# Kernel optimization log

Hardware: AMD Instinct MI355X
Metric: run time of the kernel (lower is better)

## Reference

```python
import math
import jax, jax.numpy as jnp
import numpy as np

B, T, D, L, E = 2, 1024, 1024, 12, 4
EPS = 1e-5


def _ln(v, g, b):
    mu = jnp.mean(v, axis=-1, keepdims=True)
    var = jnp.mean(jnp.square(v - mu), axis=-1, keepdims=True)
    return (v - mu) * jax.lax.rsqrt(var + EPS) * g + b


def setup_inputs() -> dict:
    key = jax.random.key(0)
    ks = jax.random.split(key, 4)
    x = jax.random.normal(ks[0], (B, T, D), dtype=jnp.float32)
    queries = jax.random.normal(ks[1], (L, D), dtype=jnp.float32) * 0.02
    W1 = jax.random.normal(ks[2], (L, D, E * D), dtype=jnp.float32) * 0.02
    W2 = jax.random.normal(ks[3], (L, E * D, D), dtype=jnp.float32) * 0.02
    return {
        'x': x,
        'queries': queries,
        'kn_g': jnp.ones((L, D), jnp.float32),
        'kn_b': jnp.zeros((L, D), jnp.float32),
        'ln_g': jnp.ones((L, D), jnp.float32),
        'ln_b': jnp.zeros((L, D), jnp.float32),
        'W1': W1,
        'b1': jnp.zeros((L, E * D), jnp.float32),
        'W2': W2,
        'b2': jnp.zeros((L, D), jnp.float32),
    }


def reference(x, queries, kn_g, kn_b, ln_g, ln_b, W1, b1, W2, b2):
    scale = 1.0 / math.sqrt(D)
    history = [x]
    h = x
    for l in range(L):
        V = jnp.stack(history, axis=0)              # (l+1, B, T, D)
        K = _ln(V, kn_g[l], kn_b[l])
        scores = jnp.einsum('d,lbtd->lbt', queries[l], K) * scale
        alpha = jax.nn.softmax(scores, axis=0)       # softmax over history axis
        residual = jnp.einsum('lbt,lbtd->btd', alpha, V)
        u = _ln(h, ln_g[l], ln_b[l])
        ff = jax.nn.gelu(u @ W1[l] + b1[l], approximate=False) @ W2[l] + b2[l]
        h = residual + ff
        history.append(h)
    return h
```

## Files before the change

kernel.cpp:

```cpp
#include <hip/hip_runtime.h>
#include <math.h>

#define BATCH 2
#define TSEQ 1024
#define DIM 1024
#define NLAYER 12
#define EDIM 4096
#define BT 2048
#define EPS_LN 1e-5f

typedef __attribute__((ext_vector_type(4))) float  f32x4;
typedef __attribute__((ext_vector_type(8))) __bf16 bf16x8;
typedef __attribute__((ext_vector_type(4))) __bf16 bf16x4;

__device__ __forceinline__ void gl_lds16(const void* gptr, void* lptr) {
    __builtin_amdgcn_global_load_lds(
        (const __attribute__((address_space(1))) void*)gptr,
        (__attribute__((address_space(3))) void*)lptr,
        16, 0, 0);
}

__device__ __forceinline__ void wtile256(float (*t)[65], const float* src,
                                         __bf16* dst, int R, int C,
                                         int rt, int ct, int tid)
{
    int lr = tid >> 2, cs = (tid & 3) << 4;
    const float* sp = src + (size_t)(rt * 64 + lr) * C + ct * 64 + cs;
#pragma unroll
    for (int s = 0; s < 4; s++) {
        f32x4 v = *(const f32x4*)(sp + s * 4);
        t[lr][cs + s * 4 + 0] = v[0];
        t[lr][cs + s * 4 + 1] = v[1];
        t[lr][cs + s * 4 + 2] = v[2];
        t[lr][cs + s * 4 + 3] = v[3];
    }
    __syncthreads();
    int oc = tid >> 2, rs = (tid & 3) << 4;
    bf16x8 o0, o1;
#pragma unroll
    for (int e = 0; e < 8; e++) o0[e] = (__bf16)t[rs + e][oc];
#pragma unroll
    for (int e = 0; e < 8; e++) o1[e] = (__bf16)t[rs + 8 + e][oc];
    __bf16* dp = dst + (size_t)(ct * 64 + oc) * R + rt * 64 + rs;
    *(bf16x8*)dp = o0;
    *(bf16x8*)(dp + 8) = o1;
}

__global__ __launch_bounds__(256) void wtrans_kernel(
    const float* __restrict__ W1, const float* __restrict__ W2,
    __bf16* __restrict__ W1t, __bf16* __restrict__ W2t)
{
    __shared__ float t[64][65];
    int z = blockIdx.z;
    if (z == 0) wtile256(t, W1, W1t, DIM, EDIM, blockIdx.y, blockIdx.x, threadIdx.x);
    else        wtile256(t, W2, W2t, EDIM, DIM, blockIdx.x, blockIdx.y, threadIdx.x);
}

__global__ __launch_bounds__(256)
void attn_wt_kernel(const float* __restrict__ x,
                    const float* __restrict__ baseprev,
                    __bf16* __restrict__ histbf,
                    const __bf16* __restrict__ part,
                    const float* __restrict__ q,
                    const float* __restrict__ kng,
                    const float* __restrict__ knb,
                    const float* __restrict__ lng,
                    const float* __restrict__ lnb,
                    const float* __restrict__ b2,
                    float* __restrict__ hnext,
                    __bf16* __restrict__ u,
                    int nl,
                    const float* __restrict__ W1n,
                    const float* __restrict__ W2n,
                    __bf16* __restrict__ W1tn,
                    __bf16* __restrict__ W2tn,
                    int dowt)
{
    __shared__ char smem[49408];

    if (blockIdx.x >= BT) {
        if (!dowt) return;
        float (*t)[65] = (float(*)[65])smem;
        int tile = blockIdx.x - BT;
        if (tile < 1024) wtile256(t, W1n, W1tn, DIM, EDIM, tile >> 6, tile & 63, threadIdx.x);
        else { int t3 = tile - 1024; wtile256(t, W2n, W2tn, EDIM, DIM, t3 & 63, t3 >> 6, threadIdx.x); }
        return;
    }

    float (*V)[DIM] = (float(*)[DIM])smem;
    float* sS  = (float*)(smem + 49152);
    float* sMu = sS + NLAYER;
    float* sRs = sMu + NLAYER;

    const int bt = blockIdx.x;
    const int tid = threadIdx.x, lane = tid & 63, w = tid >> 6;

    f32x4 gqv[4];
    float sg = 0.f, sb = 0.f;
#pragma unroll
    for (int i = 0; i < 4; i++) {
        int d = i * 256 + lane * 4;
        f32x4 g4 = *(const f32x4*)(kng + d);
        f32x4 q4 = *(const f32x4*)(q + d);
        f32x4 b4 = *(const f32x4*)(knb + d);
#pragma unroll
        for (int c = 0; c < 4; c++) {
            float gq = g4[c] * q4[c];
            gqv[i][c] = gq;
            sg += gq;
            sb += b4[c] * q4[c];
        }
    }
#pragma unroll
    for (int off = 32; off; off >>= 1) {
        sg += __shfl_xor(sg, off);
        sb += __shfl_xor(sb, off);
    }

    for (int lp = w; lp < nl; lp += 4) {
        f32x4 vv[4];
        if (lp == nl - 1) {
            const float* vp = (nl == 1) ? (x + (size_t)bt * DIM)
                                        : (baseprev + (size_t)bt * DIM);
#pragma unroll
            for (int i = 0; i < 4; i++) vv[i] = *(const f32x4*)(vp + i * 256 + lane * 4);
            if (part) {
#pragma unroll
                for (int z = 0; z < 4; z++) {
                    const __bf16* pp = part + ((size_t)z * BT + bt) * DIM;
#pragma unroll
                    for (int i = 0; i < 4; i++) {
                        bf16x4 p4 = *(const bf16x4*)(pp + i * 256 + lane * 4);
#pragma unroll
                        for (int c = 0; c < 4; c++) vv[i][c] += (float)p4[c];
                    }
                }
            }
            if (nl < NLAYER) {
                __bf16* mp = histbf + ((size_t)lp * BT + bt) * DIM;
#pragma unroll
                for (int i = 0; i < 4; i++) {
                    bf16x4 m4;
#pragma unroll
                    for (int c = 0; c < 4; c++) m4[c] = (__bf16)vv[i][c];
                    *(bf16x4*)(mp + i * 256 + lane * 4) = m4;
                }
            }
        } else {
            const __bf16* mp = histbf + ((size_t)lp * BT + bt) * DIM;
#pragma unroll
            for (int i = 0; i < 4; i++) {
                bf16x4 m4 = *(const bf16x4*)(mp + i * 256 + lane * 4);
#pragma unroll
                for (int c = 0; c < 4; c++) vv[i][c] = (float)m4[c];
            }
        }

        float s1 = 0.f, s2 = 0.f, sq = 0.f;
#pragma unroll
        for (int i = 0; i < 4; i++) {
            *(f32x4*)(&V[lp][i * 256 + lane * 4]) = vv[i];
#pragma unroll
            for (int c = 0; c < 4; c++) {
                float xv = vv[i][c];
                s1 += xv; s2 += xv * xv; sq += xv * gqv[i][c];
            }
        }
#pragma unroll
        for (int off = 32; off; off >>= 1) {
            s1 += __shfl_xor(s1, off);
            s2 += __shfl_xor(s2, off);
            sq += __shfl_xor(sq, off);
        }
        if (lane == 0) {
            float mu = s1 * (1.0f / DIM);
            float var = s2 * (1.0f / DIM) - mu * mu;
            float rs = rsqrtf(var + EPS_LN);
            sMu[lp] = mu; sRs[lp] = rs;
            sS[lp] = (rs * (sq - mu * sg) + sb) * (1.0f / 32.0f);
        }
    }
    __syncthreads();

    float mx = -1e30f;
#pragma unroll
    for (int i = 0; i < NLAYER; i++) if (i < nl) mx = fmaxf(mx, sS[i]);
    float al[NLAYER];
    float ssum = 0.f;
#pragma unroll
    for (int i = 0; i < NLAYER; i++) {
        al[i] = (i < nl) ? __expf(sS[i] - mx) : 0.f;
        ssum += al[i];
    }
    float inv = 1.0f / ssum;

    const int d = tid * 4;
    f32x4 r; r[0] = 0.f; r[1] = 0.f; r[2] = 0.f; r[3] = 0.f;
#pragma unroll
    for (int i = 0; i < NLAYER; i++) {
        if (i < nl) {
            f32x4 v4 = *(const f32x4*)(&V[i][d]);
            float a = al[i] * inv;
            r[0] += a * v4[0]; r[1] += a * v4[1]; r[2] += a * v4[2]; r[3] += a * v4[3];
        }
    }
    f32x4 h4 = *(const f32x4*)(&V[nl - 1][d]);
    f32x4 b24 = *(const f32x4*)(b2 + d);
    f32x4 ro; ro[0] = r[0] + b24[0]; ro[1] = r[1] + b24[1];
    ro[2] = r[2] + b24[2]; ro[3] = r[3] + b24[3];
    *(f32x4*)(hnext + (size_t)bt * DIM + d) = ro;

    float mu = sMu[nl - 1], rs = sRs[nl - 1];
    f32x4 g4 = *(const f32x4*)(lng + d);
    f32x4 b4 = *(const f32x4*)(lnb + d);
    bf16x4 uo;
#pragma unroll
    for (int c = 0; c < 4; c++) uo[c] = (__bf16)((h4[c] - mu) * rs * g4[c] + b4[c]);
    *(bf16x4*)(u + (size_t)bt * DIM + d) = uo;
}

#define STG 49152

template <int EPI>
__global__ __launch_bounds__(512, 1)
void gemm8(const __bf16* __restrict__ A, const __bf16* __restrict__ Bt,
           const float* __restrict__ bias, void* __restrict__ outp,
           int N, int As, int Bs)
{
    __shared__ char lds[3 * STG];
    const int tid = threadIdx.x, lane = tid & 63, w = tid >> 6;
    const int wm = w >> 2, wn = w & 3;
    const int lr = lane & 15;
    const int hib = (lane >> 4) << 4;
    const int NT = 16;

    const int fid = blockIdx.x;
    const int m0 = (fid & 15) * 128;
    const int n0 = (fid >> 4) * 256;
    const int kbase = blockIdx.y * 1024;

    f32x4 acc[4][4];
#pragma unroll
    for (int i = 0; i < 4; i++)
#pragma unroll
        for (int j = 0; j < 4; j++) { acc[i][j][0]=0.f; acc[i][j][1]=0.f; acc[i][j][2]=0.f; acc[i][j][3]=0.f; }

    const int srow = tid >> 3;
    const int ksrc = ((tid & 7) << 4) ^ ((srow & 7) << 4);
    const char* Ac = (const char*)A;
    const char* Bc = (const char*)Bt;
    size_t aoff[2], boff[4];
#pragma unroll
    for (int c = 0; c < 2; c++)
        aoff[c] = ((size_t)(m0 + c * 64 + srow) * As + kbase) * 2 + ksrc;
#pragma unroll
    for (int c = 0; c < 4; c++)
        boff[c] = ((size_t)(n0 + c * 64 + srow) * Bs + kbase) * 2 + ksrc;

    char* abw = lds + w * 1024;
    char* bbw = lds + 16384 + w * 1024;

    auto STAGE = [&](int tt, int bi) {
        size_t kb = (size_t)tt * 128;
        char* ab = abw + bi * STG;
        char* bb = bbw + bi * STG;
#pragma unroll
        for (int c = 0; c < 2; c++) gl_lds16(Ac + aoff[c] + kb, ab + c * 8192);
#pragma unroll
        for (int c = 0; c < 4; c++) gl_lds16(Bc + boff[c] + kb, bb + c * 8192);
    };

    STAGE(0, 0);
    STAGE(1, 1);

    int sb = 0, st = 2;
#pragma unroll 1
    for (int t = 0; t < NT; ++t) {
        if (t < NT - 1) asm volatile("s_waitcnt vmcnt(6)" ::: "memory");
        else            asm volatile("s_waitcnt vmcnt(0)" ::: "memory");
        __builtin_amdgcn_s_barrier();
        __builtin_amdgcn_sched_barrier(0);

        if (t + 2 < NT) STAGE(t + 2, st);

        const char* base = lds + sb * STG;
        bf16x8 af[2][4], bfr[2][4];
#pragma unroll
        for (int kk = 0; kk < 2; kk++) {
#pragma unroll
            for (int i = 0; i < 4; i++) {
                int ra = wm * 64 + i * 16 + lr;
                af[kk][i] = *(const bf16x8*)(base + ra * 128 + ((kk * 64 + hib) ^ ((ra & 7) << 4)));
            }
#pragma unroll
            for (int j = 0; j < 4; j++) {
                int rb = wn * 64 + j * 16 + lr;
                bfr[kk][j] = *(const bf16x8*)(base + 16384 + rb * 128 + ((kk * 64 + hib) ^ ((rb & 7) << 4)));
            }
        }
        __builtin_amdgcn_s_setprio(1);
#pragma unroll
        for (int kk = 0; kk < 2; kk++)
#pragma unroll
            for (int i = 0; i < 4; i++)
#pragma unroll
                for (int j = 0; j < 4; j++)
                    acc[i][j] = __builtin_amdgcn_mfma_f32_16x16x32_bf16(af[kk][i], bfr[kk][j], acc[i][j], 0, 0, 0);
        __builtin_amdgcn_s_setprio(0);

        sb = (sb == 2) ? 0 : sb + 1;
        st = (st == 2) ? 0 : st + 1;
    }

    const int lrow = (lane >> 4) << 2;
    if (EPI == 0) {
        __bf16* out = (__bf16*)outp;
#pragma unroll
        for (int i = 0; i < 4; i++) {
#pragma unroll
            for (int j = 0; j < 4; j++) {
                int colg = n0 + wn * 64 + j * 16 + lr;
                float bc = bias[colg];
#pragma unroll
                for (int r = 0; r < 4; r++) {
                    int rowg = m0 + wm * 64 + i * 16 + lrow + r;
                    float v = acc[i][j][r] + bc;
                    float tt2 = 0.7978845608f * (v + 0.044715f * v * v * v);
                    float e = __expf(2.0f * tt2);
                    float th = 1.0f - 2.0f / (e + 1.0f);
                    out[(size_t)rowg * N + colg] = (__bf16)(0.5f * v * (1.0f + th));
                }
            }
        }
    } else {
        __bf16* out = (__bf16*)outp + (size_t)blockIdx.y * BT * N;
#pragma unroll
        for (int i = 0; i < 4; i++) {
#pragma unroll
            for (int j = 0; j < 4; j++) {
                int colg = n0 + wn * 64 + j * 16 + lr;
#pragma unroll
                for (int r = 0; r < 4; r++) {
                    int rowg = m0 + wm * 64 + i * 16 + lrow + r;
                    out[(size_t)rowg * N + colg] = (__bf16)acc[i][j][r];
                }
            }
        }
    }
}

__global__ void final_reduce(const float* __restrict__ base,
                             const __bf16* __restrict__ part,
                             float* __restrict__ out)
{
    size_t i = ((size_t)blockIdx.x * 256 + threadIdx.x) * 4;
    f32x4 r = *(const f32x4*)(base + i);
#pragma unroll
    for (int z = 0; z < 4; z++) {
        bf16x4 p = *(const bf16x4*)(part + (size_t)z * BT * DIM + i);
#pragma unroll
        for (int c = 0; c < 4; c++) r[c] += (float)p[c];
    }
    *(f32x4*)(out + i) = r;
}

extern "C" void kernel_launch(void* const* d_in, const int* in_sizes, int n_in,
                              void* d_out, int out_size, void* d_ws, size_t ws_size,
                              hipStream_t stream)
{
    const float* x   = (const float*)d_in[0];
    const float* q   = (const float*)d_in[1];
    const float* kng = (const float*)d_in[2];
    const float* knb = (const float*)d_in[3];
    const float* lng = (const float*)d_in[4];
    const float* lnb = (const float*)d_in[5];
    const float* W1  = (const float*)d_in[6];
    const float* b1  = (const float*)d_in[7];
    const float* W2  = (const float*)d_in[8];
    const float* b2  = (const float*)d_in[9];

    char* ws = (char*)d_ws;
    const size_t MB = 1048576;
    float*  base2[2] = { (float*)(ws), (float*)(ws + 8 * MB) };
    __bf16* histbf = (__bf16*)(ws + 16 * MB);
    __bf16* ubuf   = (__bf16*)(ws + 64 * MB);
    __bf16* hmid   = (__bf16*)(ws + 68 * MB);
    __bf16* W1tb[2] = { (__bf16*)(ws + 84 * MB), (__bf16*)(ws + 92 * MB) };
    __bf16* W2tb[2] = { (__bf16*)(ws + 100 * MB), (__bf16*)(ws + 108 * MB) };
    __bf16* part   = (__bf16*)(ws + 116 * MB);

    wtrans_kernel<<<dim3(64, 16, 2), 256, 0, stream>>>(W1, W2, W1tb[0], W2tb[0]);

    for (int l = 0; l < NLAYER; l++) {
        int nl = l + 1;
        int ln = (l + 1 < NLAYER) ? l + 1 : l;
        float* hnext = base2[l & 1];
        const float* bprev = base2[(l + 1) & 1];
        attn_wt_kernel<<<dim3(2 * BT), 256, 0, stream>>>(
            x, bprev, histbf, (l >= 1) ? part : (const __bf16*)nullptr,
            q + (size_t)l * DIM,
            kng + (size_t)l * DIM, knb + (size_t)l * DIM,
            lng + (size_t)l * DIM, lnb + (size_t)l * DIM,
            b2 + (size_t)l * DIM, hnext, ubuf, nl,
            W1 + (size_t)ln * DIM * EDIM, W2 + (size_t)ln * EDIM * DIM,
            W1tb[(l + 1) & 1], W2tb[(l + 1) & 1], (l + 1 < NLAYER) ? 1 : 0);
        gemm8<0><<<dim3(256, 1), 512, 0, stream>>>(
            ubuf, W1tb[l & 1], b1 + (size_t)l * EDIM, (void*)hmid, EDIM, DIM, DIM);
        gemm8<2><<<dim3(64, 4), 512, 0, stream>>>(
            hmid, W2tb[l & 1], nullptr, (void*)part, DIM, EDIM, EDIM);
    }

    final_reduce<<<dim3(BT * DIM / 1024), 256, 0, stream>>>(
        base2[1], part, (float*)d_out);
}
```

Before: 897.0 us.

## Enlarge GEMM tiles to 256x256 with K32 slot-major LDS layout

Replaces the 128x256 tile GEMM, which stages a 128-wide K slab per step, with a 256x256 tile kernel that stages 32-wide K steps into a slot-major LDS layout without XOR swizzle. Each warp now owns 128x64 outputs, and A fragments are loaded in two halves to limit register pressure. The larger tile raises arithmetic intensity per byte loaded, but the grid halves to 128 blocks per GEMM, fewer than the 256 CUs. That leaves many CUs idle and doubles the number of barrier-synchronised steps.

```diff
diff --git a/kernel.cpp b/kernel.cpp
--- a/kernel.cpp
+++ b/kernel.cpp
@@ -219,55 +219,51 @@
     *(bf16x4*)(u + (size_t)bt * DIM + d) = uo;
 }
 
-#define STG 49152
-
 template <int EPI>
 __global__ __launch_bounds__(512, 1)
-void gemm8(const __bf16* __restrict__ A, const __bf16* __restrict__ Bt,
-           const float* __restrict__ bias, void* __restrict__ outp,
-           int N, int As, int Bs)
-{
-    __shared__ char lds[3 * STG];
+void gemmK32(const __bf16* __restrict__ A, const __bf16* __restrict__ Bt,
+             const float* __restrict__ bias, void* __restrict__ outp,
+             int N, int As, int Bs, int NTM)
+{
+    __shared__ char lds[98304];
     const int tid = threadIdx.x, lane = tid & 63, w = tid >> 6;
     const int wm = w >> 2, wn = w & 3;
     const int lr = lane & 15;
-    const int hib = (lane >> 4) << 4;
-    const int NT = 16;
+    const int slot = lane >> 4;
+    const int NSTEP = 32;
 
     const int fid = blockIdx.x;
-    const int m0 = (fid & 15) * 128;
-    const int n0 = (fid >> 4) * 256;
+    const int m0 = (fid % NTM) * 256;
+    const int n0 = (fid / NTM) * 256;
     const int kbase = blockIdx.y * 1024;
 
-    f32x4 acc[4][4];
-#pragma unroll
-    for (int i = 0; i < 4; i++)
+    f32x4 acc[8][4];
+#pragma unroll
+    for (int i = 0; i < 8; i++)
 #pragma unroll
         for (int j = 0; j < 4; j++) { acc[i][j][0]=0.f; acc[i][j][1]=0.f; acc[i][j][2]=0.f; acc[i][j][3]=0.f; }
 
-    const int srow = tid >> 3;
-    const int ksrc = ((tid & 7) << 4) ^ ((srow & 7) << 4);
     const char* Ac = (const char*)A;
     const char* Bc = (const char*)Bt;
-    size_t aoff[2], boff[4];
-#pragma unroll
-    for (int c = 0; c < 2; c++)
-        aoff[c] = ((size_t)(m0 + c * 64 + srow) * As + kbase) * 2 + ksrc;
-#pragma unroll
-    for (int c = 0; c < 4; c++)
-        boff[c] = ((size_t)(n0 + c * 64 + srow) * Bs + kbase) * 2 + ksrc;
-
-    char* abw = lds + w * 1024;
-    char* bbw = lds + 16384 + w * 1024;
+    size_t ag[2], bg[2];
+    int al2[2], bl2[2];
+#pragma unroll
+    for (int qq = 0; qq < 2; qq++) {
+        int idx = 2 * w + qq;
+        int rg = idx & 3, sl = idx >> 2;
+        ag[qq] = ((size_t)(m0 + rg * 64 + lane) * As + kbase) * 2 + sl * 16;
+        bg[qq] = ((size_t)(n0 + rg * 64 + lane) * Bs + kbase) * 2 + sl * 16;
+        al2[qq] = sl * 4096 + rg * 1024;
+        bl2[qq] = 16384 + sl * 4096 + rg * 1024;
+    }
 
     auto STAGE = [&](int tt, int bi) {
-        size_t kb = (size_t)tt * 128;
-        char* ab = abw + bi * STG;
-        char* bb = bbw + bi * STG;
-#pragma unroll
-        for (int c = 0; c < 2; c++) gl_lds16(Ac + aoff[c] + kb, ab + c * 8192);
-#pragma unroll
-        for (int c = 0; c < 4; c++) gl_lds16(Bc + boff[c] + kb, bb + c * 8192);
+        size_t kb = (size_t)tt * 64;
+        char* bb = lds + bi * 32768;
+#pragma unroll
+        for (int qq = 0; qq < 2; qq++) gl_lds16(Ac + ag[qq] + kb, bb + al2[qq]);
+#pragma unroll
+        for (int qq = 0; qq < 2; qq++) gl_lds16(Bc + bg[qq] + kb, bb + bl2[qq]);
     };
 
     STAGE(0, 0);
@@ -275,37 +271,39 @@
 
     int sb = 0, st = 2;
 #pragma unroll 1
-    for (int t = 0; t < NT; ++t) {
-        if (t < NT - 1) asm volatile("s_waitcnt vmcnt(6)" ::: "memory");
-        else            asm volatile("s_waitcnt vmcnt(0)" ::: "memory");
+    for (int t = 0; t < NSTEP; ++t) {
+        if (t < NSTEP - 1) asm volatile("s_waitcnt vmcnt(4)" ::: "memory");
+        else               asm volatile("s_waitcnt vmcnt(0)" ::: "memory");
         __builtin_amdgcn_s_barrier();
         __builtin_amdgcn_sched_barrier(0);
 
-        if (t + 2 < NT) STAGE(t + 2, st);
-
-        const char* base = lds + sb * STG;
-        bf16x8 af[2][4], bfr[2][4];
-#pragma unroll
-        for (int kk = 0; kk < 2; kk++) {
-#pragma unroll
-            for (int i = 0; i < 4; i++) {
-                int ra = wm * 64 + i * 16 + lr;
-                af[kk][i] = *(const bf16x8*)(base + ra * 128 + ((kk * 64 + hib) ^ ((ra & 7) << 4)));
-            }
-#pragma unroll
-            for (int j = 0; j < 4; j++) {
-                int rb = wn * 64 + j * 16 + lr;
-                bfr[kk][j] = *(const bf16x8*)(base + 16384 + rb * 128 + ((kk * 64 + hib) ^ ((rb & 7) << 4)));
-            }
-        }
+        if (t + 2 < NSTEP) STAGE(t + 2, st);
+
+        const char* aB = lds + sb * 32768 + slot * 4096;
+        const char* bB = aB + 16384;
+        bf16x8 bfr[4], afr[4];
+#pragma unroll
+        for (int j = 0; j < 4; j++)
+            bfr[j] = *(const bf16x8*)(bB + (wn * 64 + j * 16 + lr) * 16);
+#pragma unroll
+        for (int i2 = 0; i2 < 4; i2++)
+            afr[i2] = *(const bf16x8*)(aB + (wm * 128 + i2 * 16 + lr) * 16);
         __builtin_amdgcn_s_setprio(1);
 #pragma unroll
-        for (int kk = 0; kk < 2; kk++)
-#pragma unroll
-            for (int i = 0; i < 4; i++)
-#pragma unroll
-                for (int j = 0; j < 4; j++)
-                    acc[i][j] = __builtin_amdgcn_mfma_f32_16x16x32_bf16(af[kk][i], bfr[kk][j], acc[i][j], 0, 0, 0);
+        for (int i2 = 0; i2 < 4; i2++)
+#pragma unroll
+            for (int j = 0; j < 4; j++)
+                acc[i2][j] = __builtin_amdgcn_mfma_f32_16x16x32_bf16(afr[i2], bfr[j], acc[i2][j], 0, 0, 0);
+        __builtin_amdgcn_s_setprio(0);
+#pragma unroll
+        for (int i2 = 0; i2 < 4; i2++)
+            afr[i2] = *(const bf16x8*)(aB + (wm * 128 + (i2 + 4) * 16 + lr) * 16);
+        __builtin_amdgcn_s_setprio(1);
+#pragma unroll
+        for (int i2 = 0; i2 < 4; i2++)
+#pragma unroll
+            for (int j = 0; j < 4; j++)
+                acc[i2 + 4][j] = __builtin_amdgcn_mfma_f32_16x16x32_bf16(afr[i2], bfr[j], acc[i2 + 4][j], 0, 0, 0);
         __builtin_amdgcn_s_setprio(0);
 
         sb = (sb == 2) ? 0 : sb + 1;
@@ -316,14 +314,14 @@
     if (EPI == 0) {
         __bf16* out = (__bf16*)outp;
 #pragma unroll
-        for (int i = 0; i < 4; i++) {
+        for (int i = 0; i < 8; i++) {
 #pragma unroll
             for (int j = 0; j < 4; j++) {
                 int colg = n0 + wn * 64 + j * 16 + lr;
                 float bc = bias[colg];
 #pragma unroll
                 for (int r = 0; r < 4; r++) {
-                    int rowg = m0 + wm * 64 + i * 16 + lrow + r;
+                    int rowg = m0 + wm * 128 + i * 16 + lrow + r;
                     float v = acc[i][j][r] + bc;
                     float tt2 = 0.7978845608f * (v + 0.044715f * v * v * v);
                     float e = __expf(2.0f * tt2);
@@ -335,13 +333,13 @@
     } else {
         __bf16* out = (__bf16*)outp + (size_t)blockIdx.y * BT * N;
 #pragma unroll
-        for (int i = 0; i < 4; i++) {
+        for (int i = 0; i < 8; i++) {
 #pragma unroll
             for (int j = 0; j < 4; j++) {
                 int colg = n0 + wn * 64 + j * 16 + lr;
 #pragma unroll
                 for (int r = 0; r < 4; r++) {
-                    int rowg = m0 + wm * 64 + i * 16 + lrow + r;
+                    int rowg = m0 + wm * 128 + i * 16 + lrow + r;
                     out[(size_t)rowg * N + colg] = (__bf16)acc[i][j][r];
                 }
             }
@@ -404,10 +402,12 @@
             b2 + (size_t)l * DIM, hnext, ubuf, nl,
             W1 + (size_t)ln * DIM * EDIM, W2 + (size_t)ln * EDIM * DIM,
             W1tb[(l + 1) & 1], W2tb[(l + 1) & 1], (l + 1 < NLAYER) ? 1 : 0);
-        gemm8<0><<<dim3(256, 1), 512, 0, stream>>>(
-            ubuf, W1tb[l & 1], b1 + (size_t)l * EDIM, (void*)hmid, EDIM, DIM, DIM);
-        gemm8<2><<<dim3(64, 4), 512, 0, stream>>>(
-            hmid, W2tb[l & 1], nullptr, (void*)part, DIM, EDIM, EDIM);
+        gemmK32<0><<<dim3(128, 1), 512, 0, stream>>>(
+            ubuf, W1tb[l & 1], b1 + (size_t)l * EDIM, (void*)hmid,
+            EDIM, DIM, DIM, 8);
+        gemmK32<2><<<dim3(32, 4), 512, 0, stream>>>(
+            hmid, W2tb[l & 1], nullptr, (void*)part,
+            DIM, EDIM, EDIM, 8);
     }
 
     final_reduce<<<dim3(BT * DIM / 1024), 256, 0, stream>>>(
```

Result: slower. 1.468 ms (+63.6%).
